# Optimization experiments

Hardware: AMD Instinct MI355X
Metric: run time of the kernel (lower is better)

## Reference

```python
import jax, jax.numpy as jnp
import numpy as np

HEADS = 8


def _conv1d(x, w, b, pad, groups):
    # x: (N, C, L), w: (O, C//groups, K), b: (O,)
    y = jax.lax.conv_general_dilated(
        x, w, window_strides=(1,), padding=[(pad, pad)],
        dimension_numbers=("NCH", "OIH", "NCH"), feature_group_count=groups)
    return y + b[None, :, None]


def _dsconv(x, dw, db, pw, pb, pad):
    # depthwise (groups = in_channels) then 1x1 pointwise
    c = x.shape[1]
    return _conv1d(_conv1d(x, dw, db, pad, c), pw, pb, 0, 1)


def setup_inputs() -> dict:
    key = jax.random.key(0)
    b, c, l, h = 4, 64, 2048, HEADS
    ks = [3, 15]
    names_shapes = [
        ("x", (b, c, l)),
        ("q_dw", (c, 1, 1)), ("q_db", (c,)), ("q_pw", (c * h, c, 1)), ("q_pb", (c * h,)),
        ("k_dw", (c, 1, 1)), ("k_db", (c,)), ("k_pw", (c * h, c, 1)), ("k_pb", (c * h,)),
        ("v_dw", (c, 1, 1)), ("v_db", (c,)), ("v_pw", (c * h, c, 1)), ("v_pb", (c * h,)),
        ("dc0_dw", (c, 1, ks[0])), ("dc0_db", (c,)), ("dc0_pw", (c, c, 1)), ("dc0_pb", (c,)),
        ("dc1_dw", (c, 1, ks[1])), ("dc1_db", (c,)), ("dc1_pw", (c, c, 1)), ("dc1_pb", (c,)),
        ("gate", (2,)),
        ("u_w", (c, h * c * 2, 1)), ("u_b", (c,)),
    ]
    out = {}
    for i, (name, shape) in enumerate(names_shapes):
        k = jax.random.fold_in(key, i)
        scale = 1.0 if name == "x" else 0.05
        out[name] = jax.random.normal(k, shape, dtype=jnp.float32) * scale
    out["gate"] = jnp.full((2,), 0.5, dtype=jnp.float32)
    return out


def reference(x, q_dw, q_db, q_pw, q_pb, k_dw, k_db, k_pw, k_pb,
              v_dw, v_db, v_pw, v_pb,
              dc0_dw, dc0_db, dc0_pw, dc0_pb,
              dc1_dw, dc1_db, dc1_pw, dc1_pb,
              gate, u_w, u_b):
    b, c, l = x.shape
    h = HEADS
    queries = _dsconv(x, q_dw, q_db, q_pw, q_pb, 0).reshape(b * h, c, l)
    keys = _dsconv(x, k_dw, k_db, k_pw, k_pb, 0).reshape(b * h, c, l)
    values = _dsconv(x, v_dw, v_db, v_pw, v_pb, 0).reshape(b * h, c, l)

    scale = c ** (-0.25)
    # dot[bh, l_k, l_q] = keys^T @ queries; softmax over key axis (dim=1)
    dot = jnp.einsum("bck,bcq->bkq", keys * scale, queries * scale)
    attn = jax.nn.softmax(dot, axis=1)
    out = jnp.einsum("bck,bkq->bcq", values, attn).reshape(b, h * c, l)

    # dynamic multi-kernel depthwise-separable branch on values
    d0 = _dsconv(values, dc0_dw, dc0_db, dc0_pw, dc0_pb, 1)   # k=3, pad=1
    d1 = _dsconv(values, dc1_dw, dc1_db, dc1_pw, dc1_pb, 7)   # k=15, pad=7
    g = jax.nn.softmax(gate)
    dyn = (d0 * g[0] + d1 * g[1]).reshape(b, h * c, l)

    cat = jnp.concatenate([out, dyn], axis=1)  # (b, 2*h*c, l)
    # unify_heads: 1x1 conv
    return jnp.einsum("oc,bcl->bol", u_w[:, :, 0], cat) + u_b[None, :, None]
```

## Files before the change

### kernel.cpp

```cpp
#include <hip/hip_runtime.h>

typedef unsigned short u16;
typedef __attribute__((ext_vector_type(8))) short short8;
typedef __attribute__((ext_vector_type(4))) float f32x4;
typedef __attribute__((ext_vector_type(4))) u16 ushort4t;
typedef __attribute__((ext_vector_type(8))) u16 ushort8t;
typedef __attribute__((ext_vector_type(2))) unsigned uint2t;

#define MFMA16(a,b,c) __builtin_amdgcn_mfma_f32_16x16x32_bf16((a),(b),(c),0,0,0)

#define GLD16(gp, lp) __builtin_amdgcn_global_load_lds( \
    (__attribute__((address_space(1))) void*)(gp), \
    (__attribute__((address_space(3))) void*)(lp), 16, 0, 0)

__device__ __forceinline__ u16 f2bf(float f){
  unsigned u = __float_as_uint(f);
  u += 0x7FFFu + ((u>>16)&1u);
  return (u16)(u>>16);
}
__device__ __forceinline__ float bf2f(u16 h){
  return __uint_as_float(((unsigned)h)<<16);
}
__device__ __forceinline__ unsigned cvtpk(float a, float b){
  unsigned r; asm("v_cvt_pk_bf16_f32 %0, %1, %2" : "=v"(r) : "v"(a), "v"(b));
  return r;
}

#define NB 4
#define NH 8
#define CD 64
#define LS 2048
#define NBH 32
#define NPOS 8192
#define NOCH 1536

#define O_WB    0x000000
#define O_BEFF  0x040000
#define O_UWB   0x050000
#define O_WCB   0x080000
#define O_BDYN  0x090000
#define O_XT    0x100000
#define O_QT    0x200000
#define O_KT    0xA00000
#define O_VB    0x1200000
#define O_AB    0x2A00000
#define O_DB    0x3200000

__global__ __launch_bounds__(256) void prep_kernel(
    const float* qdw, const float* qdb, const float* qpw, const float* qpb,
    const float* kdw, const float* kdb, const float* kpw, const float* kpb,
    const float* vdw, const float* vdb, const float* vpw, const float* vpb,
    const float* c0pw, const float* c0db, const float* c0pb,
    const float* c1pw, const float* c1db, const float* c1pb,
    const float* gate, const float* uw,
    u16* Wb, float* beff, u16* uwb, u16* Wcb, float* bdyn)
{
  int tid = blockIdx.x*256 + threadIdx.x;
  float gm = fmaxf(gate[0], gate[1]);
  float e0 = __expf(gate[0]-gm), e1 = __expf(gate[1]-gm);
  float g0 = e0/(e0+e1), g1 = e1/(e0+e1);
  if (tid < 98304){
    int o = tid>>6, c = tid&63;
    int p = o>>9, orr = o&511;
    const float* pw = (p==0)? qpw : (p==1)? kpw : vpw;
    const float* dw = (p==0)? qdw : (p==1)? kdw : vdw;
    float v = pw[orr*64+c]*dw[c];
    if (p==0) v *= 0.125f;
    Wb[tid] = f2bf(v);
  } else if (tid < 99840){
    int o = tid - 98304;
    int p = o>>9, orr = o&511;
    const float* pw = (p==0)? qpw : (p==1)? kpw : vpw;
    const float* db = (p==0)? qdb : (p==1)? kdb : vdb;
    const float* pb = (p==0)? qpb : (p==1)? kpb : vpb;
    float s = pb[orr];
    for (int c=0;c<64;++c) s += pw[orr*64+c]*db[c];
    if (p==0) s *= 0.125f;
    beff[o] = s;
  } else if (tid < 165376){
    int i = tid - 99840;
    uwb[i] = f2bf(uw[i]);
  } else if (tid < 173568){
    int i = tid - 165376;
    int o = i>>7, c2 = i&127, k = c2>>6, c = c2&63;
    float wv = k ? (g1*c1pw[o*64+c]) : (g0*c0pw[o*64+c]);
    Wcb[i] = f2bf(wv);
  } else if (tid < 173632){
    int o = tid - 173568;
    float s = g0*c0pb[o] + g1*c1pb[o];
    for (int c=0;c<64;++c) s += g0*c0pw[o*64+c]*c0db[c] + g1*c1pw[o*64+c]*c1db[c];
    bdyn[o] = s;
  }
}

__global__ __launch_bounds__(256) void transpose_kernel(const float* x, u16* xt){
  __shared__ float tile[64][65];
  int t = threadIdx.x;
  int l0 = blockIdx.x*64, b = blockIdx.y;
  #pragma unroll
  for (int j=0;j<4;++j){
    int fl = t + j*256;
    int c = fl>>4, qd = fl&15;
    f32x4 v = *(const f32x4*)(x + ((size_t)(b*64+c))*LS + l0 + qd*4);
    tile[c][qd*4+0]=v[0]; tile[c][qd*4+1]=v[1]; tile[c][qd*4+2]=v[2]; tile[c][qd*4+3]=v[3];
  }
  __syncthreads();
  int l = t>>2, cg = t&3;
  ushort8t a, bv;
  #pragma unroll
  for (int j=0;j<8;++j) a[j] = f2bf(tile[cg*16+j][l]);
  #pragma unroll
  for (int j=0;j<8;++j) bv[j] = f2bf(tile[cg*16+8+j][l]);
  u16* dst = xt + ((size_t)(b*LS + l0 + l))*64 + cg*16;
  *(ushort8t*)dst = a;
  *(ushort8t*)(dst+8) = bv;
}

__global__ __launch_bounds__(256) void proj_kernel(const u16* Wb, const float* beff, const u16* xt,
    u16* Qt, u16* Kt, u16* Vb)
{
  int tid = threadIdx.x, w = tid>>6, lane = tid&63;
  int q16 = lane&15, g = lane>>4;
  int o0 = blockIdx.y*128 + (w>>1)*64;
  int p0 = blockIdx.x*128 + (w&1)*64;
  short8 af[4][2], bfr[4][2];
  #pragma unroll
  for (int mt=0;mt<4;++mt)
    #pragma unroll
    for (int s=0;s<2;++s)
      af[mt][s] = *(const short8*)(Wb + (size_t)(o0+mt*16+q16)*64 + s*32 + g*8);
  #pragma unroll
  for (int nt=0;nt<4;++nt)
    #pragma unroll
    for (int s=0;s<2;++s)
      bfr[nt][s] = *(const short8*)(xt + (size_t)(p0+nt*16+q16)*64 + s*32 + g*8);
  f32x4 acc[4][4];
  #pragma unroll
  for (int mt=0;mt<4;++mt)
    #pragma unroll
    for (int nt=0;nt<4;++nt) acc[mt][nt] = (f32x4){0.f,0.f,0.f,0.f};
  #pragma unroll
  for (int s=0;s<2;++s)
    #pragma unroll
    for (int mt=0;mt<4;++mt)
      #pragma unroll
      for (int nt=0;nt<4;++nt)
        acc[mt][nt] = MFMA16(af[mt][s], bfr[nt][s], acc[mt][nt]);
  #pragma unroll
  for (int mt=0;mt<4;++mt){
    int obase = o0 + mt*16;
    int p = obase>>9;
    int h = (obase>>6)&7;
    int c0 = (obase&63) + g*4;
    f32x4 bvv = *(const f32x4*)(beff + obase + g*4);
    #pragma unroll
    for (int nt=0;nt<4;++nt){
      int pos = p0 + nt*16 + q16;
      int b = pos>>11, l = pos&2047;
      int bh = b*8 + h;
      float v0 = acc[mt][nt][0]+bvv[0], v1 = acc[mt][nt][1]+bvv[1],
            v2 = acc[mt][nt][2]+bvv[2], v3 = acc[mt][nt][3]+bvv[3];
      if (p==0){
        ushort4t pk = {f2bf(v0),f2bf(v1),f2bf(v2),f2bf(v3)};
        *(ushort4t*)(Qt + ((size_t)(bh*LS+l))*64 + c0) = pk;
      } else if (p==1){
        ushort4t pk = {f2bf(v0),f2bf(v1),f2bf(v2),f2bf(v3)};
        *(ushort4t*)(Kt + ((size_t)(bh*LS+l))*64 + c0) = pk;
      } else {
        size_t base = ((size_t)(bh*64+c0))*LS + l;
        Vb[base]      = f2bf(v0);
        Vb[base+LS]   = f2bf(v1);
        Vb[base+2*LS] = f2bf(v2);
        Vb[base+3*LS] = f2bf(v3);
      }
    }
  }
}

__global__ __launch_bounds__(128) void attn_kernel(const u16* Qt, const u16* Kt, const u16* Vb, u16* Ab)
{
  __shared__ __align__(16) char lds[40960];
  const int tid = threadIdx.x;
  const int w = tid>>6, lane = tid&63;
  const int q16 = lane&15, g = lane>>4;
  const int bh = blockIdx.y;
  const int q0 = blockIdx.x*64 + w*32;
  char* ldsK = lds;
  char* ldsV = lds + 16384;
  char* ldsP = lds + 32768 + w*4096;

  short8 qf[2][2];
  #pragma unroll
  for (int qg=0;qg<2;++qg){
    const u16* qb = Qt + ((size_t)(bh*LS + q0 + qg*16 + q16))*64 + g*8;
    qf[qg][0] = *(const short8*)qb;
    qf[qg][1] = *(const short8*)(qb + 32);
  }

  float mrun[2] = {-1e30f,-1e30f}, lrun[2] = {0.f,0.f};
  f32x4 oacc[2][4];
  #pragma unroll
  for (int qg=0;qg<2;++qg)
    #pragma unroll
    for (int i=0;i<4;++i) oacc[qg][i] = (f32x4){0.f,0.f,0.f,0.f};

  const int chunk = lane&7, rsub = lane>>3;
  const int swzq = q16&7;

  #pragma unroll
  for (int r2=0;r2<4;++r2){
    int row = w*32 + r2*8 + rsub;
    int sch = chunk ^ (row&7);
    GLD16(Kt + ((size_t)(bh*LS + row))*64 + sch*8, ldsK + row*128 + chunk*16);
    GLD16(Vb + ((size_t)(bh*64 + row))*LS + sch*8, ldsV + row*128 + chunk*16);
  }

  int cur = 0;
  for (int kt=0; kt<32; ++kt){
    if (kt+1 < 32){
      int k0 = (kt+1)*64;
      #pragma unroll
      for (int r2=0;r2<4;++r2){
        int row = w*32 + r2*8 + rsub;
        int sch = chunk ^ (row&7);
        GLD16(Kt + ((size_t)(bh*LS + k0 + row))*64 + sch*8,
              ldsK + (cur^1)*8192 + row*128 + chunk*16);
        GLD16(Vb + ((size_t)(bh*64 + row))*LS + k0 + sch*8,
              ldsV + (cur^1)*8192 + row*128 + chunk*16);
      }
      asm volatile("s_waitcnt vmcnt(8)" ::: "memory");
    } else {
      asm volatile("s_waitcnt vmcnt(0)" ::: "memory");
    }
    __builtin_amdgcn_s_barrier();
    char* lK = ldsK + cur*8192;
    char* lV = ldsV + cur*8192;

    f32x4 s[2][4];
    #pragma unroll
    for (int qg=0;qg<2;++qg)
      #pragma unroll
      for (int i=0;i<4;++i) s[qg][i] = (f32x4){0.f,0.f,0.f,0.f};
    __builtin_amdgcn_s_setprio(1);
    #pragma unroll
    for (int ss=0; ss<2; ++ss){
      #pragma unroll
      for (int mt=0; mt<4; ++mt){
        short8 kf = *(short8*)(lK + (mt*16+q16)*128 + (((ss*4+g)^swzq)<<4));
        s[0][mt] = MFMA16(kf, qf[0][ss], s[0][mt]);
        s[1][mt] = MFMA16(kf, qf[1][ss], s[1][mt]);
      }
    }
    __builtin_amdgcn_s_setprio(0);

    #pragma unroll
    for (int qg=0;qg<2;++qg){
      float tmax = -1e30f;
      #pragma unroll
      for (int mt=0;mt<4;++mt)
        tmax = fmaxf(tmax, fmaxf(fmaxf(s[qg][mt][0],s[qg][mt][1]), fmaxf(s[qg][mt][2],s[qg][mt][3])));
      tmax = fmaxf(tmax, __shfl_xor(tmax,16));
      tmax = fmaxf(tmax, __shfl_xor(tmax,32));
      if (__any(tmax > mrun[qg])){
        float mnew = fmaxf(mrun[qg], tmax);
        float corr = __expf(mrun[qg] - mnew);
        lrun[qg] *= corr;
        #pragma unroll
        for (int i=0;i<4;++i) oacc[qg][i] *= corr;
        mrun[qg] = mnew;
      }
      float ps = 0.f;
      #pragma unroll
      for (int mt=0;mt<4;++mt){
        #pragma unroll
        for (int r=0;r<4;++r){
          float p = __expf(s[qg][mt][r]-mrun[qg]);
          s[qg][mt][r] = p; ps += p;
        }
      }
      ps += __shfl_xor(ps,16);
      ps += __shfl_xor(ps,32);
      lrun[qg] += ps;

      #pragma unroll
      for (int mt=0;mt<4;++mt){
        uint2t pk = { cvtpk(s[qg][mt][0], s[qg][mt][1]),
                      cvtpk(s[qg][mt][2], s[qg][mt][3]) };
        int cw = (2*mt + (g>>1)) ^ swzq;
        *(uint2t*)(ldsP + qg*2048 + q16*128 + (cw<<4) + (g&1)*8) = pk;
      }
    }

    __builtin_amdgcn_s_setprio(1);
    #pragma unroll
    for (int half=0; half<2; ++half){
      short8 pf0 = *(short8*)(ldsP +        q16*128 + (((half*4+g)^swzq)<<4));
      short8 pf1 = *(short8*)(ldsP + 2048 + q16*128 + (((half*4+g)^swzq)<<4));
      #pragma unroll
      for (int ct=0;ct<4;++ct){
        short8 vf = *(short8*)(lV + (ct*16+q16)*128 + (((half*4+g)^swzq)<<4));
        oacc[0][ct] = MFMA16(vf, pf0, oacc[0][ct]);
        oacc[1][ct] = MFMA16(vf, pf1, oacc[1][ct]);
      }
    }
    __builtin_amdgcn_s_setprio(0);
    __builtin_amdgcn_s_barrier();
    cur ^= 1;
  }
  #pragma unroll
  for (int qg=0;qg<2;++qg){
    float inv = 1.f/lrun[qg];
    u16* ab = Ab + ((size_t)(bh*LS + q0 + qg*16 + q16))*64;
    #pragma unroll
    for (int ct=0;ct<4;++ct){
      ushort4t ov = {f2bf(oacc[qg][ct][0]*inv),f2bf(oacc[qg][ct][1]*inv),
                     f2bf(oacc[qg][ct][2]*inv),f2bf(oacc[qg][ct][3]*inv)};
      *(ushort4t*)(ab + ct*16 + g*4) = ov;
    }
  }
}

__global__ __launch_bounds__(256) void dyn_kernel(const u16* Vb, const float* d0w, const float* d1w,
    const u16* Wcb, const float* bdyn, u16* Db)
{
  __shared__ __align__(16) u16 Y[16384];
  const int t = threadIdx.x;
  const int bh = blockIdx.y;
  const int l0 = blockIdx.x*128;
  const int c = t>>2, sub = t&3;
  const int base = l0 + sub*32 - 8;
  const u16* vrow = Vb + (size_t)(bh*64 + c)*LS;

  u16 vwin[48];
  if (base >= 0 && base + 48 <= 2048){
    #pragma unroll
    for (int k=0;k<6;++k)
      *(ushort8t*)(vwin + k*8) = *(const ushort8t*)(vrow + base + k*8);
  } else {
    #pragma unroll
    for (int k=0;k<48;++k){
      int gi = base + k;
      vwin[k] = ((unsigned)gi < 2048u) ? vrow[gi] : (u16)0;
    }
  }
  float fw[48];
  #pragma unroll
  for (int k=0;k<48;++k) fw[k] = bf2f(vwin[k]);
  float w1[15], w0[3];
  #pragma unroll
  for (int k=0;k<15;++k) w1[k] = d1w[c*15+k];
  #pragma unroll
  for (int k=0;k<3;++k)  w0[k] = d0w[c*3+k];

  const int chi = c>>3, clo = c&7;
  #pragma unroll
  for (int j=0;j<32;++j){
    float a1 = 0.f;
    #pragma unroll
    for (int k=0;k<15;++k) a1 += fw[j+1+k]*w1[k];
    float a0 = fw[j+7]*w0[0] + fw[j+8]*w0[1] + fw[j+9]*w0[2];
    int lloc = sub*32 + j;
    int swl = lloc&7;
    Y[lloc*128 + (chi^swl)*8 + clo]     = f2bf(a0);
    Y[lloc*128 + ((8+chi)^swl)*8 + clo] = f2bf(a1);
  }
  __syncthreads();

  const int w = t>>6, lane = t&63;
  const int q16 = lane&15, g = lane>>4;
  short8 af[4][4];
  #pragma unroll
  for (int mt=0;mt<4;++mt)
    #pragma unroll
    for (int ks=0;ks<4;++ks)
      af[mt][ks] = *(const short8*)(Wcb + (mt*16+q16)*128 + ks*32 + g*8);
  f32x4 acc[4][2];
  #pragma unroll
  for (int mt=0;mt<4;++mt){ acc[mt][0]=(f32x4){0.f,0.f,0.f,0.f}; acc[mt][1]=(f32x4){0.f,0.f,0.f,0.f}; }
  #pragma unroll
  for (int ks=0;ks<4;++ks){
    #pragma unroll
    for (int nt=0;nt<2;++nt){
      int pos = w*32 + nt*16 + q16;
      int ch = (ks*4+g) ^ (pos&7);
      short8 bf = *(const short8*)(&Y[pos*128 + ch*8]);
      #pragma unroll
      for (int mt=0;mt<4;++mt)
        acc[mt][nt] = MFMA16(af[mt][ks], bf, acc[mt][nt]);
    }
  }
  #pragma unroll
  for (int mt=0;mt<4;++mt){
    f32x4 bv = *(const f32x4*)(bdyn + mt*16 + g*4);
    #pragma unroll
    for (int nt=0;nt<2;++nt){
      int pos = l0 + w*32 + nt*16 + q16;
      ushort4t pk = {f2bf(acc[mt][nt][0]+bv[0]), f2bf(acc[mt][nt][1]+bv[1]),
                     f2bf(acc[mt][nt][2]+bv[2]), f2bf(acc[mt][nt][3]+bv[3])};
      *(ushort4t*)(Db + ((size_t)(bh*LS+pos))*64 + mt*16 + g*4) = pk;
    }
  }
}

__global__ __launch_bounds__(256) void unify_kernel(const u16* uwb, const float* ub,
    const u16* Ab, const u16* Db, float* out)
{
  __shared__ f32x4 red[3][4][64];
  int tid = threadIdx.x, kh = tid>>6, lane = tid&63;
  int q16 = lane&15, g = lane>>4;
  int pos = blockIdx.x*16 + q16;
  int b = pos>>11, pl = pos&2047;
  f32x4 acc[4];
  #pragma unroll
  for (int i=0;i<4;++i) acc[i]=(f32x4){0.f,0.f,0.f,0.f};
  #pragma unroll
  for (int i=0;i<8;++i){
    int ks = kh*8 + i;
    int ch = ks*32 + g*8;
    const u16* src;
    if (ks < 16){
      src = Ab + ((size_t)((b*8 + (ch>>6))*LS + pl))*64 + (ch&63);
    } else {
      int c2 = ch - 512;
      src = Db + ((size_t)((b*8 + (c2>>6))*LS + pl))*64 + (c2&63);
    }
    short8 bf = *(const short8*)src;
    #pragma unroll
    for (int mt=0;mt<4;++mt){
      short8 af = *(const short8*)(uwb + (size_t)(mt*16+q16)*1024 + ks*32 + g*8);
      acc[mt] = MFMA16(af, bf, acc[mt]);
    }
  }
  if (kh > 0){
    #pragma unroll
    for (int mt=0;mt<4;++mt) red[kh-1][mt][lane] = acc[mt];
  }
  __syncthreads();
  if (kh == 0){
    #pragma unroll
    for (int mt=0;mt<4;++mt){
      f32x4 a = acc[mt];
      a += red[0][mt][lane];
      a += red[1][mt][lane];
      a += red[2][mt][lane];
      #pragma unroll
      for (int r=0;r<4;++r){
        int o = mt*16 + g*4 + r;
        out[((size_t)(b*64+o))*LS + pl] = a[r] + ub[o];
      }
    }
  }
}

extern "C" void kernel_launch(void* const* d_in, const int* in_sizes, int n_in,
                              void* d_out, int out_size, void* d_ws, size_t ws_size,
                              hipStream_t stream)
{
  const float* x    = (const float*)d_in[0];
  const float* qdw  = (const float*)d_in[1];
  const float* qdb  = (const float*)d_in[2];
  const float* qpw  = (const float*)d_in[3];
  const float* qpb  = (const float*)d_in[4];
  const float* kdw  = (const float*)d_in[5];
  const float* kdb  = (const float*)d_in[6];
  const float* kpw  = (const float*)d_in[7];
  const float* kpb  = (const float*)d_in[8];
  const float* vdw  = (const float*)d_in[9];
  const float* vdb  = (const float*)d_in[10];
  const float* vpw  = (const float*)d_in[11];
  const float* vpb  = (const float*)d_in[12];
  const float* c0dw = (const float*)d_in[13];
  const float* c0db = (const float*)d_in[14];
  const float* c0pw = (const float*)d_in[15];
  const float* c0pb = (const float*)d_in[16];
  const float* c1dw = (const float*)d_in[17];
  const float* c1db = (const float*)d_in[18];
  const float* c1pw = (const float*)d_in[19];
  const float* c1pb = (const float*)d_in[20];
  const float* gate = (const float*)d_in[21];
  const float* uw   = (const float*)d_in[22];
  const float* ubias= (const float*)d_in[23];
  float* out = (float*)d_out;
  char* ws = (char*)d_ws;

  u16*   Wb   = (u16*)(ws + O_WB);
  float* beff = (float*)(ws + O_BEFF);
  u16*   uwb  = (u16*)(ws + O_UWB);
  u16*   Wcb  = (u16*)(ws + O_WCB);
  float* bdyn = (float*)(ws + O_BDYN);
  u16*   xt   = (u16*)(ws + O_XT);
  u16*   Qt   = (u16*)(ws + O_QT);
  u16*   Kt   = (u16*)(ws + O_KT);
  u16*   Vb   = (u16*)(ws + O_VB);
  u16*   Ab   = (u16*)(ws + O_AB);
  u16*   Db   = (u16*)(ws + O_DB);

  prep_kernel<<<dim3(679), dim3(256), 0, stream>>>(
      qdw,qdb,qpw,qpb, kdw,kdb,kpw,kpb, vdw,vdb,vpw,vpb,
      c0pw,c0db,c0pb, c1pw,c1db,c1pb, gate, uw,
      Wb, beff, uwb, Wcb, bdyn);
  transpose_kernel<<<dim3(32,4), dim3(256), 0, stream>>>(x, xt);
  proj_kernel<<<dim3(64,12), dim3(256), 0, stream>>>(Wb, beff, xt, Qt, Kt, Vb);
  attn_kernel<<<dim3(32,32), dim3(128), 0, stream>>>(Qt, Kt, Vb, Ab);
  dyn_kernel<<<dim3(16,32), dim3(256), 0, stream>>>(Vb, c0dw, c1dw, Wcb, bdyn, Db);
  unify_kernel<<<dim3(512), dim3(256), 0, stream>>>(uwb, ubias, Ab, Db, out);
}
```

Before: 222.6 us.

## Widen attention blocks to four waves, fold log2e into Q, defer row-sum reductions

The attention kernel now runs 256 threads per block covering 128 queries, so each K/V tile loaded into LDS is shared by four waves instead of two. Each wave now issues 4 global-to-LDS loads per stage instead of 8. Blocks are remapped with an XCD-aware swizzle so blocks with the same bh land together for L2 reuse. The log2(e) factor is folded into the Q projection scale so exp2f replaces __expf, and the cross-lane shuffles for the running sum move to the epilogue; the max shuffles now run only when a rescale is needed. The trade-offs are half as many blocks (512) and a larger LDS footprint (48 KB) per block, which may reduce occupancy.

```diff
diff --git a/kernel.cpp b/kernel.cpp
--- a/kernel.cpp
+++ b/kernel.cpp
@@ -55,6 +55,7 @@
     const float* gate, const float* uw,
     u16* Wb, float* beff, u16* uwb, u16* Wcb, float* bdyn)
 {
+  const float QSCL = 0.125f * 1.44269504088896f;
   int tid = blockIdx.x*256 + threadIdx.x;
   float gm = fmaxf(gate[0], gate[1]);
   float e0 = __expf(gate[0]-gm), e1 = __expf(gate[1]-gm);
@@ -65,7 +66,7 @@
     const float* pw = (p==0)? qpw : (p==1)? kpw : vpw;
     const float* dw = (p==0)? qdw : (p==1)? kdw : vdw;
     float v = pw[orr*64+c]*dw[c];
-    if (p==0) v *= 0.125f;
+    if (p==0) v *= QSCL;
     Wb[tid] = f2bf(v);
   } else if (tid < 99840){
     int o = tid - 98304;
@@ -75,7 +76,7 @@
     const float* pb = (p==0)? qpb : (p==1)? kpb : vpb;
     float s = pb[orr];
     for (int c=0;c<64;++c) s += pw[orr*64+c]*db[c];
-    if (p==0) s *= 0.125f;
+    if (p==0) s *= QSCL;
     beff[o] = s;
   } else if (tid < 165376){
     int i = tid - 99840;
@@ -177,14 +178,16 @@
   }
 }
 
-__global__ __launch_bounds__(128) void attn_kernel(const u16* Qt, const u16* Kt, const u16* Vb, u16* Ab)
+__global__ __launch_bounds__(256) void attn_kernel(const u16* Qt, const u16* Kt, const u16* Vb, u16* Ab)
 {
-  __shared__ __align__(16) char lds[40960];
+  __shared__ __align__(16) char lds[49152];
   const int tid = threadIdx.x;
   const int w = tid>>6, lane = tid&63;
   const int q16 = lane&15, g = lane>>4;
-  const int bh = blockIdx.y;
-  const int q0 = blockIdx.x*64 + w*32;
+  const int bid = blockIdx.x;
+  const int sw = (bid&7)*64 + (bid>>3);
+  const int qtile = sw & 15, bh = sw >> 4;
+  const int q0 = qtile*128 + w*32;
   char* ldsK = lds;
   char* ldsV = lds + 16384;
   char* ldsP = lds + 32768 + w*4096;
@@ -204,31 +207,26 @@
     #pragma unroll
     for (int i=0;i<4;++i) oacc[qg][i] = (f32x4){0.f,0.f,0.f,0.f};
 
-  const int chunk = lane&7, rsub = lane>>3;
+  const int srow = w*8 + (lane>>3);
+  const int chunk = lane&7;
+  const int sch = chunk ^ (lane>>3);
   const int swzq = q16&7;
 
-  #pragma unroll
-  for (int r2=0;r2<4;++r2){
-    int row = w*32 + r2*8 + rsub;
-    int sch = chunk ^ (row&7);
-    GLD16(Kt + ((size_t)(bh*LS + row))*64 + sch*8, ldsK + row*128 + chunk*16);
-    GLD16(Vb + ((size_t)(bh*64 + row))*LS + sch*8, ldsV + row*128 + chunk*16);
-  }
+  GLD16(Kt + ((size_t)(bh*LS + srow))*64      + sch*8, ldsK + w*1024 + lane*16);
+  GLD16(Kt + ((size_t)(bh*LS + 32 + srow))*64 + sch*8, ldsK + 4096 + w*1024 + lane*16);
+  GLD16(Vb + ((size_t)(bh*64 + srow))*LS      + sch*8, ldsV + w*1024 + lane*16);
+  GLD16(Vb + ((size_t)(bh*64 + 32 + srow))*LS + sch*8, ldsV + 4096 + w*1024 + lane*16);
 
   int cur = 0;
   for (int kt=0; kt<32; ++kt){
     if (kt+1 < 32){
       int k0 = (kt+1)*64;
-      #pragma unroll
-      for (int r2=0;r2<4;++r2){
-        int row = w*32 + r2*8 + rsub;
-        int sch = chunk ^ (row&7);
-        GLD16(Kt + ((size_t)(bh*LS + k0 + row))*64 + sch*8,
-              ldsK + (cur^1)*8192 + row*128 + chunk*16);
-        GLD16(Vb + ((size_t)(bh*64 + row))*LS + k0 + sch*8,
-              ldsV + (cur^1)*8192 + row*128 + chunk*16);
-      }
-      asm volatile("s_waitcnt vmcnt(8)" ::: "memory");
+      int nb = (cur^1)*8192;
+      GLD16(Kt + ((size_t)(bh*LS + k0 + srow))*64      + sch*8, ldsK + nb + w*1024 + lane*16);
+      GLD16(Kt + ((size_t)(bh*LS + k0 + 32 + srow))*64 + sch*8, ldsK + nb + 4096 + w*1024 + lane*16);
+      GLD16(Vb + ((size_t)(bh*64 + srow))*LS + k0      + sch*8, ldsV + nb + w*1024 + lane*16);
+      GLD16(Vb + ((size_t)(bh*64 + 32 + srow))*LS + k0 + sch*8, ldsV + nb + 4096 + w*1024 + lane*16);
+      asm volatile("s_waitcnt vmcnt(4)" ::: "memory");
     } else {
       asm volatile("s_waitcnt vmcnt(0)" ::: "memory");
     }
@@ -255,15 +253,15 @@
 
     #pragma unroll
     for (int qg=0;qg<2;++qg){
-      float tmax = -1e30f;
-      #pragma unroll
-      for (int mt=0;mt<4;++mt)
+      float tmax = fmaxf(fmaxf(s[qg][0][0],s[qg][0][1]), fmaxf(s[qg][0][2],s[qg][0][3]));
+      #pragma unroll
+      for (int mt=1;mt<4;++mt)
         tmax = fmaxf(tmax, fmaxf(fmaxf(s[qg][mt][0],s[qg][mt][1]), fmaxf(s[qg][mt][2],s[qg][mt][3])));
-      tmax = fmaxf(tmax, __shfl_xor(tmax,16));
-      tmax = fmaxf(tmax, __shfl_xor(tmax,32));
       if (__any(tmax > mrun[qg])){
+        tmax = fmaxf(tmax, __shfl_xor(tmax,16));
+        tmax = fmaxf(tmax, __shfl_xor(tmax,32));
         float mnew = fmaxf(mrun[qg], tmax);
-        float corr = __expf(mrun[qg] - mnew);
+        float corr = exp2f(mrun[qg] - mnew);
         lrun[qg] *= corr;
         #pragma unroll
         for (int i=0;i<4;++i) oacc[qg][i] *= corr;
@@ -274,12 +272,10 @@
       for (int mt=0;mt<4;++mt){
         #pragma unroll
         for (int r=0;r<4;++r){
-          float p = __expf(s[qg][mt][r]-mrun[qg]);
+          float p = exp2f(s[qg][mt][r]-mrun[qg]);
           s[qg][mt][r] = p; ps += p;
         }
       }
-      ps += __shfl_xor(ps,16);
-      ps += __shfl_xor(ps,32);
       lrun[qg] += ps;
 
       #pragma unroll
@@ -309,7 +305,10 @@
   }
   #pragma unroll
   for (int qg=0;qg<2;++qg){
-    float inv = 1.f/lrun[qg];
+    float lr = lrun[qg];
+    lr += __shfl_xor(lr,16);
+    lr += __shfl_xor(lr,32);
+    float inv = 1.f/lr;
     u16* ab = Ab + ((size_t)(bh*LS + q0 + qg*16 + q16))*64;
     #pragma unroll
     for (int ct=0;ct<4;++ct){
@@ -501,7 +500,7 @@
       Wb, beff, uwb, Wcb, bdyn);
   transpose_kernel<<<dim3(32,4), dim3(256), 0, stream>>>(x, xt);
   proj_kernel<<<dim3(64,12), dim3(256), 0, stream>>>(Wb, beff, xt, Qt, Kt, Vb);
-  attn_kernel<<<dim3(32,32), dim3(128), 0, stream>>>(Qt, Kt, Vb, Ab);
+  attn_kernel<<<dim3(512), dim3(256), 0, stream>>>(Qt, Kt, Vb, Ab);
   dyn_kernel<<<dim3(16,32), dim3(256), 0, stream>>>(Vb, c0dw, c1dw, Wcb, bdyn, Db);
   unify_kernel<<<dim3(512), dim3(256), 0, stream>>>(uwb, ubias, Ab, Db, out);
 }
```

Measured after the change: 224.3 us. No clear change (+0.7%).
